# Kernel tuning notes

Measured on AMD Instinct MI355X. Metric: run time of the kernel, lower is better.

The kernel has to match this reference:

```python
import jax, jax.numpy as jnp
import numpy as np

N = 100000      # nodes
E = 1600000     # edges
H = 32          # hidden_channels
G = 512         # graphs in batch
F_IN = 7        # input node feature dim (fixed by GCNConv(7, H))
RRELU_SLOPE = (1.0 / 8.0 + 1.0 / 3.0) / 2.0  # eval-mode RReLU negative slope


def _rrelu(v):
    return jnp.where(v >= 0, v, RRELU_SLOPE * v)


def _gcn(x, row, col, ew, W, b):
    # GCNConv with normalize=True, add_self_loops=False
    deg = jax.ops.segment_sum(ew, col, num_segments=N)
    dis = jnp.where(deg > 0, jax.lax.rsqrt(deg), 0.0)
    norm = dis[row] * ew * dis[col]            # [E]
    h = x @ W                                  # [N, H]
    out = jax.ops.segment_sum(norm[:, None] * h[row], col, num_segments=N)
    return out + b


def setup_inputs() -> dict:
    key = jax.random.key(0)
    ks = jax.random.split(key, 12)
    s = 0.1
    x = jax.random.normal(ks[0], (N, F_IN), dtype=jnp.float32)
    edge_index = jax.random.randint(ks[1], (2, E), 0, N)
    batch = jnp.sort(jax.random.randint(ks[2], (N,), 0, G))
    edge_weights = jax.random.uniform(ks[3], (E,), dtype=jnp.float32)
    W1 = jax.random.normal(ks[4], (F_IN, H), dtype=jnp.float32) * s
    b1 = jnp.zeros((H,), jnp.float32)
    W2 = jax.random.normal(ks[5], (H, H), dtype=jnp.float32) * s
    b2 = jnp.zeros((H,), jnp.float32)
    Wl1 = jax.random.normal(ks[6], (H, H), dtype=jnp.float32) * s
    bl1 = jnp.zeros((H,), jnp.float32)
    Wl2 = jax.random.normal(ks[7], (H, H), dtype=jnp.float32) * s
    bl2 = jnp.zeros((H,), jnp.float32)
    Wl3 = jax.random.normal(ks[8], (H, 1), dtype=jnp.float32) * s
    bl3 = jnp.zeros((1,), jnp.float32)
    return dict(x=x, edge_index=edge_index, batch=batch, edge_weights=edge_weights,
                W1=W1, b1=b1, W2=W2, b2=b2, Wl1=Wl1, bl1=bl1, Wl2=Wl2, bl2=bl2,
                Wl3=Wl3, bl3=bl3)


def reference(x, edge_index, batch, edge_weights, W1, b1, W2, b2,
              Wl1, bl1, Wl2, bl2, Wl3, bl3):
    row, col = edge_index[0], edge_index[1]
    # conv1 (weighted GCN)
    x = _gcn(x, row, col, edge_weights, W1, b1)
    # max_pool_neighbor_x: max over incoming neighbors + self-loop
    self_idx = jnp.arange(N)
    x = jax.ops.segment_max(
        jnp.concatenate([x[row], x], axis=0),
        jnp.concatenate([col, self_idx], axis=0),
        num_segments=N)
    res = x
    # conv2 (unit edge weights)
    ones_ew = jnp.ones((E,), x.dtype)
    x = _gcn(x, row, col, ones_ew, W2, b2)
    x = jax.nn.relu(res + x)
    # global max pool over graphs
    x = jax.ops.segment_max(x, batch, num_segments=G)   # [G, H]
    res = x
    x = x @ Wl1 + bl1
    x = _rrelu(res + x)
    res = x
    x = x @ Wl2 + bl2
    x = _rrelu(res + x)
    # dropout: identity in eval mode
    x = x @ Wl3 + bl3
    return _rrelu(x)                                     # [G, 1]
```

## Files before the change

### kernel.cpp

```cpp
#include <hip/hip_runtime.h>
#include <hip/hip_bf16.h>

#define NN 100000
#define EE 1600000
#define HH 32
#define GG 512
#define FIN 7
#define NBUK 391
#define EPB 2048
#define P1G 782
#define BCAP 4608
#define SLOPE 0.22916666666666666f
#define QS 32767.0f
#define IQS (1.0f / 32767.0f)
#define RMASK 0x1FFFFu

typedef unsigned short bf16_t;
typedef unsigned int uint32;

__device__ __forceinline__ bf16_t f2b(float f) {
    return (bf16_t)(__bfloat16_as_ushort(__float2bfloat16(f)));
}
__device__ __forceinline__ float b2f(bf16_t u) {
    return __uint_as_float(((uint32)u) << 16);
}
__device__ __forceinline__ float lo16(uint32 u) { return __uint_as_float(u << 16); }
__device__ __forceinline__ float hi16(uint32 u) { return __uint_as_float(u & 0xFFFF0000u); }
__device__ __forceinline__ uint32 pack2(float a, float b) {
    return (uint32)f2b(a) | ((uint32)f2b(b) << 16);
}

__global__ __launch_bounds__(256) void k_p1(const int* __restrict__ row,
                                            const int* __restrict__ col,
                                            const float* __restrict__ ew,
                                            int* __restrict__ gcur,
                                            uint32* __restrict__ pay,
                                            unsigned char* __restrict__ nlo) {
    __shared__ int hist[NBUK];
    __shared__ int base[NBUK];
    int t = threadIdx.x;
    for (int i = t; i < NBUK; i += 256) hist[i] = 0;
    __syncthreads();
    int e0 = blockIdx.x * EPB;
    int e1 = min(e0 + EPB, EE);
    for (int e = e0 + t; e < e1; e += 256) atomicAdd(&hist[col[e] >> 8], 1);
    __syncthreads();
    for (int i = t; i < NBUK; i += 256) {
        int h = hist[i];
        base[i] = h > 0 ? atomicAdd(&gcur[i], h) : 0;
        hist[i] = 0;
    }
    __syncthreads();
    for (int e = e0 + t; e < e1; e += 256) {
        int c = col[e];
        int b = c >> 8;
        int r = atomicAdd(&hist[b], 1);
        int idx = base[b] + r;
        if (idx < BCAP) {
            size_t pos = (size_t)b * BCAP + idx;
            uint32 q = (uint32)(ew[e] * QS + 0.5f);
            pay[pos] = (q << 17) | (uint32)row[e];
            nlo[pos] = (unsigned char)(c & 255);
        }
    }
}

__global__ __launch_bounds__(512) void k_scanb(const int* __restrict__ gcur,
                                               int* __restrict__ gbase) {
    __shared__ int s[512];
    int t = threadIdx.x;
    int v = (t < NBUK) ? min(gcur[t], BCAP) : 0;
    s[t] = v;
    __syncthreads();
#pragma unroll
    for (int d = 1; d < 512; d <<= 1) {
        int u = (t >= d) ? s[t - d] : 0;
        __syncthreads();
        s[t] += u;
        __syncthreads();
    }
    if (t < NBUK) gbase[t] = s[t] - v;
}

__global__ __launch_bounds__(256) void k_p2(const int* __restrict__ gcur,
                                            const int* __restrict__ gbase,
                                            const uint32* __restrict__ pay,
                                            const unsigned char* __restrict__ nlo,
                                            const float* __restrict__ x,
                                            uint32* __restrict__ spack,
                                            int* __restrict__ cnt,
                                            int* __restrict__ off,
                                            float* __restrict__ d1s,
                                            float* __restrict__ d2,
                                            uint32* __restrict__ xsu) {
    __shared__ int hist[256];
    __shared__ int s[256];
    __shared__ int cur[256];
    __shared__ int qsum[256];
    int b = blockIdx.x, t = threadIdx.x;
    int M = min(gcur[b], BCAP);
    const uint32* bp = pay + (size_t)b * BCAP;
    const unsigned char* bn = nlo + (size_t)b * BCAP;
    hist[t] = 0;
    qsum[t] = 0;
    __syncthreads();
    for (int j = t; j < M; j += 256) atomicAdd(&hist[bn[j]], 1);
    __syncthreads();
    int v = hist[t];
    s[t] = v;
    __syncthreads();
#pragma unroll
    for (int d = 1; d < 256; d <<= 1) {
        int u = (t >= d) ? s[t - d] : 0;
        __syncthreads();
        s[t] += u;
        __syncthreads();
    }
    int excl = s[t] - v;
    int gb = gbase[b];
    int n = b * 256 + t;
    if (n < NN) { cnt[n] = v; off[n] = gb + excl; }
    cur[t] = excl;
    __syncthreads();
    for (int j = t; j < M; j += 256) {
        uint32 p = bp[j];
        unsigned char nb = bn[j];
        int r = atomicAdd(&cur[nb], 1);
        spack[gb + r] = p;
        atomicAdd(&qsum[nb], (int)(p >> 17));
    }
    __syncthreads();
    if (n < NN) {
        int sq = qsum[t];
        float dis1 = sq > 0 ? rsqrtf((float)sq * IQS) : 0.0f;
        d1s[n] = dis1 * IQS;
        d2[n] = v > 0 ? rsqrtf((float)v) : 0.0f;
        float f0 = x[n * FIN + 0] * dis1, f1 = x[n * FIN + 1] * dis1;
        float f2 = x[n * FIN + 2] * dis1, f3 = x[n * FIN + 3] * dis1;
        float f4 = x[n * FIN + 4] * dis1, f5 = x[n * FIN + 5] * dis1;
        float f6 = x[n * FIN + 6] * dis1;
        xsu[n * 4 + 0] = pack2(f0, f1);
        xsu[n * 4 + 1] = pack2(f2, f3);
        xsu[n * 4 + 2] = pack2(f4, f5);
        xsu[n * 4 + 3] = pack2(f6, 0.0f);
    }
}

__global__ __launch_bounds__(256) void k_agg1(const int* __restrict__ off,
                                              const int* __restrict__ cnt,
                                              const uint32* __restrict__ spack,
                                              const uint4* __restrict__ XS,
                                              const float* __restrict__ d1s,
                                              const float* __restrict__ b1,
                                              const float* __restrict__ W1,
                                              uint32* __restrict__ x1u) {
    __shared__ float sW[FIN * HH];
    int t = threadIdx.x;
    if (t < FIN * HH) sW[t] = W1[t];
    __syncthreads();
    int n = blockIdx.x * 16 + (t >> 4);
    int l = t & 15;
    int o = off[n], m = cnt[n];
    const uint32* bin = spack + o;
    float a0 = 0, a1 = 0, a2 = 0, a3 = 0, a4 = 0, a5 = 0, a6 = 0;
    for (int j = l; j < m; j += 16) {
        uint32 p = bin[j];
        uint4 v = XS[p & RMASK];
        float q = (float)(p >> 17);
        a0 += q * lo16(v.x); a1 += q * hi16(v.x);
        a2 += q * lo16(v.y); a3 += q * hi16(v.y);
        a4 += q * lo16(v.z); a5 += q * hi16(v.z);
        a6 += q * lo16(v.w);
    }
#pragma unroll
    for (int q = 8; q >= 1; q >>= 1) {
        a0 += __shfl_xor(a0, q, 16); a1 += __shfl_xor(a1, q, 16);
        a2 += __shfl_xor(a2, q, 16); a3 += __shfl_xor(a3, q, 16);
        a4 += __shfl_xor(a4, q, 16); a5 += __shfl_xor(a5, q, 16);
        a6 += __shfl_xor(a6, q, 16);
    }
    float sc = d1s[n];
    int c0 = 2 * l, c1 = 2 * l + 1;
    float s0 = a0 * sW[c0] + a1 * sW[HH + c0] + a2 * sW[2 * HH + c0]
             + a3 * sW[3 * HH + c0] + a4 * sW[4 * HH + c0]
             + a5 * sW[5 * HH + c0] + a6 * sW[6 * HH + c0];
    float s1 = a0 * sW[c1] + a1 * sW[HH + c1] + a2 * sW[2 * HH + c1]
             + a3 * sW[3 * HH + c1] + a4 * sW[4 * HH + c1]
             + a5 * sW[5 * HH + c1] + a6 * sW[6 * HH + c1];
    x1u[n * 16 + l] = pack2(sc * s0 + b1[c0], sc * s1 + b1[c1]);
}

__global__ __launch_bounds__(256) void k_pool(const int* __restrict__ off,
                                              const int* __restrict__ cnt,
                                              const uint32* __restrict__ spack,
                                              const uint32* __restrict__ X1,
                                              const float* __restrict__ d2,
                                              uint32* __restrict__ xpu,
                                              uint32* __restrict__ xpsu) {
    int t = threadIdx.x;
    int n = blockIdx.x * 16 + (t >> 4);
    int cp = t & 15;
    int o = off[n], m = cnt[n];
    const uint32* bin = spack + o;
    uint32 self = X1[n * 16 + cp];
    float m0 = lo16(self), m1 = hi16(self);
    int j = 0;
    for (; j + 3 < m; j += 4) {
        uint32 u0 = X1[(bin[j] & RMASK) * 16 + cp];
        uint32 u1 = X1[(bin[j + 1] & RMASK) * 16 + cp];
        uint32 u2 = X1[(bin[j + 2] & RMASK) * 16 + cp];
        uint32 u3 = X1[(bin[j + 3] & RMASK) * 16 + cp];
        m0 = fmaxf(fmaxf(m0, lo16(u0)), fmaxf(lo16(u1), fmaxf(lo16(u2), lo16(u3))));
        m1 = fmaxf(fmaxf(m1, hi16(u0)), fmaxf(hi16(u1), fmaxf(hi16(u2), hi16(u3))));
    }
    for (; j < m; j++) {
        uint32 u0 = X1[(bin[j] & RMASK) * 16 + cp];
        m0 = fmaxf(m0, lo16(u0));
        m1 = fmaxf(m1, hi16(u0));
    }
    float dn = d2[n];
    xpu[n * 16 + cp] = pack2(m0, m1);
    xpsu[n * 16 + cp] = pack2(dn * m0, dn * m1);
}

__global__ __launch_bounds__(256) void k_agg2(const int* __restrict__ off,
                                              const int* __restrict__ cnt,
                                              const uint32* __restrict__ spack,
                                              const uint32* __restrict__ XPS,
                                              float2* __restrict__ SO) {
    int t = threadIdx.x;
    int n = blockIdx.x * 16 + (t >> 4);
    int cp = t & 15;
    int o = off[n], m = cnt[n];
    const uint32* bin = spack + o;
    float a0 = 0.0f, a1 = 0.0f;
    int j = 0;
    for (; j + 3 < m; j += 4) {
        uint32 u0 = XPS[(bin[j] & RMASK) * 16 + cp];
        uint32 u1 = XPS[(bin[j + 1] & RMASK) * 16 + cp];
        uint32 u2 = XPS[(bin[j + 2] & RMASK) * 16 + cp];
        uint32 u3 = XPS[(bin[j + 3] & RMASK) * 16 + cp];
        a0 += lo16(u0) + lo16(u1) + lo16(u2) + lo16(u3);
        a1 += hi16(u0) + hi16(u1) + hi16(u2) + hi16(u3);
    }
    for (; j < m; j++) {
        uint32 u0 = XPS[(bin[j] & RMASK) * 16 + cp];
        a0 += lo16(u0);
        a1 += hi16(u0);
    }
    SO[n * 16 + cp] = make_float2(a0, a1);
}

__global__ __launch_bounds__(256) void k_xn(const float* __restrict__ Sf,
                                            const uint32* __restrict__ xpu,
                                            const float* __restrict__ d2,
                                            const float* __restrict__ b2,
                                            const float* __restrict__ W2,
                                            bf16_t* __restrict__ xnh) {
    __shared__ float sW[HH * HH];
    __shared__ float sx[8][HH];
    int t = threadIdx.x;
    for (int j = t; j < HH * HH; j += 256) sW[j] = W2[j];
    int n = blockIdx.x * 8 + (t >> 5);
    int c = t & 31, w = t >> 5;
    sx[w][c] = Sf[n * HH + c];
    __syncthreads();
    const float* xr = sx[w];
    float acc = 0.0f;
#pragma unroll
    for (int k = 0; k < HH; k++) acc += xr[k] * sW[k * HH + c];
    uint32 u = xpu[n * 16 + (c >> 1)];
    float xpv = (c & 1) ? hi16(u) : lo16(u);
    xnh[n * HH + c] = f2b(fmaxf(xpv + d2[n] * acc + b2[c], 0.0f));
}

__global__ __launch_bounds__(256) void k_gpool_mlp(const bf16_t* __restrict__ xnh,
                                                   const int* __restrict__ batch,
                                                   const float* __restrict__ Wl1,
                                                   const float* __restrict__ bl1,
                                                   const float* __restrict__ Wl2,
                                                   const float* __restrict__ bl2,
                                                   const float* __restrict__ Wl3,
                                                   const float* __restrict__ bl3,
                                                   float* __restrict__ out) {
    __shared__ float sW1[HH * HH];
    __shared__ float sW2[HH * HH];
    __shared__ float sW3[HH];
    __shared__ float sred[8][HH];
    int t = threadIdx.x;
    int g = blockIdx.x;
    for (int j = t; j < HH * HH; j += 256) {
        sW1[j] = Wl1[j];
        sW2[j] = Wl2[j];
    }
    if (t < HH) sW3[t] = Wl3[t];

    int lo = 0, hi = NN;
    while (lo < hi) { int mid = (lo + hi) >> 1; if (batch[mid] < g) lo = mid + 1; else hi = mid; }
    int s = lo;
    hi = NN;
    while (lo < hi) { int mid = (lo + hi) >> 1; if (batch[mid] < g + 1) lo = mid + 1; else hi = mid; }
    int e = lo;

    int c = t & 31, w = t >> 5;
    float mx = -3.0e38f;
    for (int i = s + w; i < e; i += 8) mx = fmaxf(mx, b2f(xnh[i * HH + c]));
    sred[w][c] = mx;
    __syncthreads();

    if (t < HH) {
        float x0 = sred[0][t];
#pragma unroll
        for (int q = 1; q < 8; q++) x0 = fmaxf(x0, sred[q][t]);
        float acc = 0.0f;
#pragma unroll
        for (int k = 0; k < HH; k++) acc += __shfl(x0, k, 32) * sW1[k * HH + t];
        float a1 = x0 + acc + bl1[t];
        a1 = a1 >= 0.0f ? a1 : SLOPE * a1;
        float acc2 = 0.0f;
#pragma unroll
        for (int k = 0; k < HH; k++) acc2 += __shfl(a1, k, 32) * sW2[k * HH + t];
        float a2 = a1 + acc2 + bl2[t];
        a2 = a2 >= 0.0f ? a2 : SLOPE * a2;
        float p = a2 * sW3[t];
#pragma unroll
        for (int o = 16; o >= 1; o >>= 1) p += __shfl_down(p, o, 32);
        if (t == 0) {
            float o = p + bl3[0];
            o = o >= 0.0f ? o : SLOPE * o;
            out[g] = o;
        }
    }
}

extern "C" void kernel_launch(void* const* d_in, const int* in_sizes, int n_in,
                              void* d_out, int out_size, void* d_ws, size_t ws_size,
                              hipStream_t stream) {
    const float* x   = (const float*)d_in[0];
    const int*   ei  = (const int*)d_in[1];
    const int*   bat = (const int*)d_in[2];
    const float* ew  = (const float*)d_in[3];
    const float* W1  = (const float*)d_in[4];
    const float* b1  = (const float*)d_in[5];
    const float* W2  = (const float*)d_in[6];
    const float* b2  = (const float*)d_in[7];
    const float* Wl1 = (const float*)d_in[8];
    const float* bl1 = (const float*)d_in[9];
    const float* Wl2 = (const float*)d_in[10];
    const float* bl2 = (const float*)d_in[11];
    const float* Wl3 = (const float*)d_in[12];
    const float* bl3 = (const float*)d_in[13];
    float* out = (float*)d_out;

    const int* row = ei;
    const int* col = ei + EE;

    char* w = (char*)d_ws;
    uint32* spack = (uint32*)w;  w += (size_t)EE * 4;
    uint32* pay   = (uint32*)w;  w += (size_t)NBUK * BCAP * 4;
    int*    gcur  = (int*)w;     w += NBUK * 4;
    int*    gbase = (int*)w;     w += NBUK * 4;
    int*    cnt   = (int*)w;     w += NN * 4;
    int*    off   = (int*)w;     w += NN * 4;
    float*  d1s   = (float*)w;   w += NN * 4;
    float*  d2    = (float*)w;   w += NN * 4;
    uint32* xsu   = (uint32*)w;  w += (size_t)NN * 4 * 4;
    uint32* x1u   = (uint32*)w;  w += (size_t)NN * 16 * 4;
    uint32* xpu   = (uint32*)w;  w += (size_t)NN * 16 * 4;
    uint32* xpsu  = (uint32*)w;  w += (size_t)NN * 16 * 4;
    float*  Sf    = (float*)w;   w += (size_t)NN * HH * 4;
    bf16_t* xnh   = (bf16_t*)w;  w += (size_t)NN * HH * 2;
    unsigned char* nlo = (unsigned char*)w;  w += (size_t)NBUK * BCAP;

    hipMemsetAsync(gcur, 0, NBUK * sizeof(int), stream);

    k_p1    <<<P1G, 256, 0, stream>>>(row, col, ew, gcur, pay, nlo);
    k_scanb <<<1, 512, 0, stream>>>(gcur, gbase);
    k_p2    <<<NBUK, 256, 0, stream>>>(gcur, gbase, pay, nlo, x, spack, cnt, off, d1s, d2, xsu);
    k_agg1  <<<NN / 16, 256, 0, stream>>>(off, cnt, spack, (const uint4*)xsu, d1s, b1, W1, x1u);
    k_pool  <<<NN / 16, 256, 0, stream>>>(off, cnt, spack, x1u, d2, xpu, xpsu);
    k_agg2  <<<NN / 16, 256, 0, stream>>>(off, cnt, spack, xpsu, (float2*)Sf);
    k_xn    <<<NN / 8, 256, 0, stream>>>(Sf, xpu, d2, b2, W2, xnh);
    k_gpool_mlp<<<GG, 256, 0, stream>>>(xnh, bat, Wl1, bl1, Wl2, bl2, Wl3, bl3, out);
}
```

Measured before the change: 275.6 us.

## Deterministic block-local binning and 16-byte wide-gather pool/agg2 kernels

The edge bucketing pass no longer takes global atomic bucket slots. Each block now sorts its edges locally by bucket into a per-block region, packing row, weight and local column into 64-bit words, and records per-block bucket offsets in a matrix. The second pass gathers each bucket's segments from every block into shared memory. This removes the memset, the scan kernel and the global atomics, but k_p2 now does serial per-segment copy loops and holds a large shared-memory array. Separately, the pool and agg2 kernels now use 64 lanes per node, each loading a 16-byte chunk for one of 16 edges, with results combined by wavefront shuffle reductions. This gives more memory-level parallelism per node, but launches four times as many blocks.

```diff
diff --git a/kernel.cpp b/kernel.cpp
--- a/kernel.cpp
+++ b/kernel.cpp
@@ -17,6 +17,7 @@
 
 typedef unsigned short bf16_t;
 typedef unsigned int uint32;
+typedef unsigned long long uint64;
 
 __device__ __forceinline__ bf16_t f2b(float f) {
     return (bf16_t)(__bfloat16_as_ushort(__float2bfloat16(f)));
@@ -33,59 +34,40 @@
 __global__ __launch_bounds__(256) void k_p1(const int* __restrict__ row,
                                             const int* __restrict__ col,
                                             const float* __restrict__ ew,
-                                            int* __restrict__ gcur,
-                                            uint32* __restrict__ pay,
-                                            unsigned char* __restrict__ nlo) {
-    __shared__ int hist[NBUK];
-    __shared__ int base[NBUK];
-    int t = threadIdx.x;
-    for (int i = t; i < NBUK; i += 256) hist[i] = 0;
-    __syncthreads();
-    int e0 = blockIdx.x * EPB;
-    int e1 = min(e0 + EPB, EE);
-    for (int e = e0 + t; e < e1; e += 256) atomicAdd(&hist[col[e] >> 8], 1);
-    __syncthreads();
-    for (int i = t; i < NBUK; i += 256) {
-        int h = hist[i];
-        base[i] = h > 0 ? atomicAdd(&gcur[i], h) : 0;
-        hist[i] = 0;
-    }
-    __syncthreads();
+                                            int* __restrict__ Pmat,
+                                            uint64* __restrict__ pay) {
+    __shared__ int h[512];
+    __shared__ int cur[392];
+    int t = threadIdx.x;
+    h[t] = 0; h[t + 256] = 0;
+    __syncthreads();
+    int e0 = blockIdx.x * EPB, e1 = min(e0 + EPB, EE);
+    for (int e = e0 + t; e < e1; e += 256) atomicAdd(&h[col[e] >> 8], 1);
+    __syncthreads();
+    int c0 = h[t], c1 = h[t + 256];
+    for (int d = 1; d < 512; d <<= 1) {
+        int a = (t >= d) ? h[t - d] : 0;
+        int b = h[t + 256 - d];
+        __syncthreads();
+        h[t] += a; h[t + 256] += b;
+        __syncthreads();
+    }
+    int ex0 = h[t] - c0, ex1 = h[t + 256] - c1;
+    if (t < 392) { cur[t] = ex0; Pmat[blockIdx.x * 392 + t] = ex0; }
+    if (t + 256 < 392) { cur[t + 256] = ex1; Pmat[blockIdx.x * 392 + t + 256] = ex1; }
+    __syncthreads();
+    uint64* bpay = pay + (size_t)blockIdx.x * EPB;
     for (int e = e0 + t; e < e1; e += 256) {
         int c = col[e];
         int b = c >> 8;
-        int r = atomicAdd(&hist[b], 1);
-        int idx = base[b] + r;
-        if (idx < BCAP) {
-            size_t pos = (size_t)b * BCAP + idx;
-            uint32 q = (uint32)(ew[e] * QS + 0.5f);
-            pay[pos] = (q << 17) | (uint32)row[e];
-            nlo[pos] = (unsigned char)(c & 255);
-        }
-    }
-}
-
-__global__ __launch_bounds__(512) void k_scanb(const int* __restrict__ gcur,
-                                               int* __restrict__ gbase) {
-    __shared__ int s[512];
-    int t = threadIdx.x;
-    int v = (t < NBUK) ? min(gcur[t], BCAP) : 0;
-    s[t] = v;
-    __syncthreads();
-#pragma unroll
-    for (int d = 1; d < 512; d <<= 1) {
-        int u = (t >= d) ? s[t - d] : 0;
-        __syncthreads();
-        s[t] += u;
-        __syncthreads();
-    }
-    if (t < NBUK) gbase[t] = s[t] - v;
-}
-
-__global__ __launch_bounds__(256) void k_p2(const int* __restrict__ gcur,
-                                            const int* __restrict__ gbase,
-                                            const uint32* __restrict__ pay,
-                                            const unsigned char* __restrict__ nlo,
+        uint32 q = (uint32)(ew[e] * QS + 0.5f);
+        int r = atomicAdd(&cur[b], 1);
+        bpay[r] = ((uint64)(uint32)(c & 255) << 32) | ((uint64)q << 17) | (uint32)row[e];
+    }
+}
+
+__global__ __launch_bounds__(256) void k_p2(const int* __restrict__ Pmat,
+                                            const uint64* __restrict__ pay,
                                             const float* __restrict__ x,
                                             uint32* __restrict__ spack,
                                             int* __restrict__ cnt,
@@ -93,23 +75,29 @@
                                             float* __restrict__ d1s,
                                             float* __restrict__ d2,
                                             uint32* __restrict__ xsu) {
-    __shared__ int hist[256];
-    __shared__ int s[256];
-    __shared__ int cur[256];
-    __shared__ int qsum[256];
+    __shared__ uint64 staged[BCAP];
+    __shared__ int hist[256], s[256], cur[256], qsum[256];
+    __shared__ int tot;
     int b = blockIdx.x, t = threadIdx.x;
-    int M = min(gcur[b], BCAP);
-    const uint32* bp = pay + (size_t)b * BCAP;
-    const unsigned char* bn = nlo + (size_t)b * BCAP;
-    hist[t] = 0;
-    qsum[t] = 0;
-    __syncthreads();
-    for (int j = t; j < M; j += 256) atomicAdd(&hist[bn[j]], 1);
-    __syncthreads();
-    int v = hist[t];
-    s[t] = v;
-    __syncthreads();
-#pragma unroll
+    hist[t] = 0; qsum[t] = 0;
+    if (t == 0) tot = 0;
+    __syncthreads();
+    for (int k = t; k < P1G; k += 256) {
+        int s0 = Pmat[k * 392 + b];
+        int s1 = Pmat[k * 392 + b + 1];
+        int len = s1 - s0;
+        if (len > 0) {
+            int r0 = atomicAdd(&tot, len);
+            const uint64* src = pay + (size_t)k * EPB + s0;
+            for (int i = 0; i < len && r0 + i < BCAP; i++) staged[r0 + i] = src[i];
+        }
+    }
+    __syncthreads();
+    int M = min(tot, BCAP);
+    for (int j = t; j < M; j += 256) atomicAdd(&hist[(int)(staged[j] >> 32)], 1);
+    __syncthreads();
+    int v = hist[t]; s[t] = v;
+    __syncthreads();
     for (int d = 1; d < 256; d <<= 1) {
         int u = (t >= d) ? s[t - d] : 0;
         __syncthreads();
@@ -117,17 +105,17 @@
         __syncthreads();
     }
     int excl = s[t] - v;
-    int gb = gbase[b];
+    int gb = b * BCAP;
     int n = b * 256 + t;
     if (n < NN) { cnt[n] = v; off[n] = gb + excl; }
     cur[t] = excl;
     __syncthreads();
     for (int j = t; j < M; j += 256) {
-        uint32 p = bp[j];
-        unsigned char nb = bn[j];
+        uint64 p = staged[j];
+        int nb = (int)(p >> 32);
         int r = atomicAdd(&cur[nb], 1);
-        spack[gb + r] = p;
-        atomicAdd(&qsum[nb], (int)(p >> 17));
+        spack[gb + r] = (uint32)p;
+        atomicAdd(&qsum[nb], (int)((uint32)p >> 17));
     }
     __syncthreads();
     if (n < NN) {
@@ -198,57 +186,83 @@
                                               uint32* __restrict__ xpu,
                                               uint32* __restrict__ xpsu) {
     int t = threadIdx.x;
-    int n = blockIdx.x * 16 + (t >> 4);
-    int cp = t & 15;
+    int n = blockIdx.x * 4 + (t >> 6);
+    int l = t & 63;
+    int eg = l >> 2, qt = l & 3;
     int o = off[n], m = cnt[n];
     const uint32* bin = spack + o;
-    uint32 self = X1[n * 16 + cp];
-    float m0 = lo16(self), m1 = hi16(self);
-    int j = 0;
-    for (; j + 3 < m; j += 4) {
-        uint32 u0 = X1[(bin[j] & RMASK) * 16 + cp];
-        uint32 u1 = X1[(bin[j + 1] & RMASK) * 16 + cp];
-        uint32 u2 = X1[(bin[j + 2] & RMASK) * 16 + cp];
-        uint32 u3 = X1[(bin[j + 3] & RMASK) * 16 + cp];
-        m0 = fmaxf(fmaxf(m0, lo16(u0)), fmaxf(lo16(u1), fmaxf(lo16(u2), lo16(u3))));
-        m1 = fmaxf(fmaxf(m1, hi16(u0)), fmaxf(hi16(u1), fmaxf(hi16(u2), hi16(u3))));
-    }
-    for (; j < m; j++) {
-        uint32 u0 = X1[(bin[j] & RMASK) * 16 + cp];
-        m0 = fmaxf(m0, lo16(u0));
-        m1 = fmaxf(m1, hi16(u0));
-    }
-    float dn = d2[n];
-    xpu[n * 16 + cp] = pack2(m0, m1);
-    xpsu[n * 16 + cp] = pack2(dn * m0, dn * m1);
+    const uint4* X4 = (const uint4*)X1;
+    uint4 u = X4[n * 4 + qt];
+    float m0 = lo16(u.x), m1 = hi16(u.x), m2 = lo16(u.y), m3 = hi16(u.y);
+    float m4 = lo16(u.z), m5 = hi16(u.z), m6 = lo16(u.w), m7 = hi16(u.w);
+    for (int j0 = 0; j0 < m; j0 += 16) {
+        int j = j0 + eg;
+        int r = (j < m) ? (int)(bin[j] & RMASK) : n;
+        uint4 v = X4[r * 4 + qt];
+        m0 = fmaxf(m0, lo16(v.x)); m1 = fmaxf(m1, hi16(v.x));
+        m2 = fmaxf(m2, lo16(v.y)); m3 = fmaxf(m3, hi16(v.y));
+        m4 = fmaxf(m4, lo16(v.z)); m5 = fmaxf(m5, hi16(v.z));
+        m6 = fmaxf(m6, lo16(v.w)); m7 = fmaxf(m7, hi16(v.w));
+    }
+#pragma unroll
+    for (int o2 = 4; o2 < 64; o2 <<= 1) {
+        m0 = fmaxf(m0, __shfl_xor(m0, o2, 64));
+        m1 = fmaxf(m1, __shfl_xor(m1, o2, 64));
+        m2 = fmaxf(m2, __shfl_xor(m2, o2, 64));
+        m3 = fmaxf(m3, __shfl_xor(m3, o2, 64));
+        m4 = fmaxf(m4, __shfl_xor(m4, o2, 64));
+        m5 = fmaxf(m5, __shfl_xor(m5, o2, 64));
+        m6 = fmaxf(m6, __shfl_xor(m6, o2, 64));
+        m7 = fmaxf(m7, __shfl_xor(m7, o2, 64));
+    }
+    if (eg == 0) {
+        float dn = d2[n];
+        uint4 w0, w1;
+        w0.x = pack2(m0, m1); w0.y = pack2(m2, m3);
+        w0.z = pack2(m4, m5); w0.w = pack2(m6, m7);
+        w1.x = pack2(dn * m0, dn * m1); w1.y = pack2(dn * m2, dn * m3);
+        w1.z = pack2(dn * m4, dn * m5); w1.w = pack2(dn * m6, dn * m7);
+        ((uint4*)xpu)[n * 4 + qt] = w0;
+        ((uint4*)xpsu)[n * 4 + qt] = w1;
+    }
 }
 
 __global__ __launch_bounds__(256) void k_agg2(const int* __restrict__ off,
                                               const int* __restrict__ cnt,
                                               const uint32* __restrict__ spack,
                                               const uint32* __restrict__ XPS,
-                                              float2* __restrict__ SO) {
-    int t = threadIdx.x;
-    int n = blockIdx.x * 16 + (t >> 4);
-    int cp = t & 15;
+                                              float* __restrict__ Sf) {
+    int t = threadIdx.x;
+    int n = blockIdx.x * 4 + (t >> 6);
+    int l = t & 63;
+    int eg = l >> 2, qt = l & 3;
     int o = off[n], m = cnt[n];
     const uint32* bin = spack + o;
-    float a0 = 0.0f, a1 = 0.0f;
-    int j = 0;
-    for (; j + 3 < m; j += 4) {
-        uint32 u0 = XPS[(bin[j] & RMASK) * 16 + cp];
-        uint32 u1 = XPS[(bin[j + 1] & RMASK) * 16 + cp];
-        uint32 u2 = XPS[(bin[j + 2] & RMASK) * 16 + cp];
-        uint32 u3 = XPS[(bin[j + 3] & RMASK) * 16 + cp];
-        a0 += lo16(u0) + lo16(u1) + lo16(u2) + lo16(u3);
-        a1 += hi16(u0) + hi16(u1) + hi16(u2) + hi16(u3);
-    }
-    for (; j < m; j++) {
-        uint32 u0 = XPS[(bin[j] & RMASK) * 16 + cp];
-        a0 += lo16(u0);
-        a1 += hi16(u0);
-    }
-    SO[n * 16 + cp] = make_float2(a0, a1);
+    const uint4* X4 = (const uint4*)XPS;
+    float a0 = 0, a1 = 0, a2 = 0, a3 = 0, a4 = 0, a5 = 0, a6 = 0, a7 = 0;
+    for (int j0 = 0; j0 < m; j0 += 16) {
+        int j = j0 + eg;
+        if (j < m) {
+            uint4 v = X4[(bin[j] & RMASK) * 4 + qt];
+            a0 += lo16(v.x); a1 += hi16(v.x);
+            a2 += lo16(v.y); a3 += hi16(v.y);
+            a4 += lo16(v.z); a5 += hi16(v.z);
+            a6 += lo16(v.w); a7 += hi16(v.w);
+        }
+    }
+#pragma unroll
+    for (int o2 = 4; o2 < 64; o2 <<= 1) {
+        a0 += __shfl_xor(a0, o2, 64); a1 += __shfl_xor(a1, o2, 64);
+        a2 += __shfl_xor(a2, o2, 64); a3 += __shfl_xor(a3, o2, 64);
+        a4 += __shfl_xor(a4, o2, 64); a5 += __shfl_xor(a5, o2, 64);
+        a6 += __shfl_xor(a6, o2, 64); a7 += __shfl_xor(a7, o2, 64);
+    }
+    if (eg == 0) {
+        float4 f0 = make_float4(a0, a1, a2, a3);
+        float4 f1 = make_float4(a4, a5, a6, a7);
+        ((float4*)Sf)[n * 8 + qt * 2] = f0;
+        ((float4*)Sf)[n * 8 + qt * 2 + 1] = f1;
+    }
 }
 
 __global__ __launch_bounds__(256) void k_xn(const float* __restrict__ Sf,
@@ -356,30 +370,25 @@
     const int* col = ei + EE;
 
     char* w = (char*)d_ws;
-    uint32* spack = (uint32*)w;  w += (size_t)EE * 4;
-    uint32* pay   = (uint32*)w;  w += (size_t)NBUK * BCAP * 4;
-    int*    gcur  = (int*)w;     w += NBUK * 4;
-    int*    gbase = (int*)w;     w += NBUK * 4;
-    int*    cnt   = (int*)w;     w += NN * 4;
-    int*    off   = (int*)w;     w += NN * 4;
-    float*  d1s   = (float*)w;   w += NN * 4;
-    float*  d2    = (float*)w;   w += NN * 4;
-    uint32* xsu   = (uint32*)w;  w += (size_t)NN * 4 * 4;
-    uint32* x1u   = (uint32*)w;  w += (size_t)NN * 16 * 4;
-    uint32* xpu   = (uint32*)w;  w += (size_t)NN * 16 * 4;
-    uint32* xpsu  = (uint32*)w;  w += (size_t)NN * 16 * 4;
-    float*  Sf    = (float*)w;   w += (size_t)NN * HH * 4;
-    bf16_t* xnh   = (bf16_t*)w;  w += (size_t)NN * HH * 2;
-    unsigned char* nlo = (unsigned char*)w;  w += (size_t)NBUK * BCAP;
-
-    hipMemsetAsync(gcur, 0, NBUK * sizeof(int), stream);
-
-    k_p1    <<<P1G, 256, 0, stream>>>(row, col, ew, gcur, pay, nlo);
-    k_scanb <<<1, 512, 0, stream>>>(gcur, gbase);
-    k_p2    <<<NBUK, 256, 0, stream>>>(gcur, gbase, pay, nlo, x, spack, cnt, off, d1s, d2, xsu);
-    k_agg1  <<<NN / 16, 256, 0, stream>>>(off, cnt, spack, (const uint4*)xsu, d1s, b1, W1, x1u);
-    k_pool  <<<NN / 16, 256, 0, stream>>>(off, cnt, spack, x1u, d2, xpu, xpsu);
-    k_agg2  <<<NN / 16, 256, 0, stream>>>(off, cnt, spack, xpsu, (float2*)Sf);
-    k_xn    <<<NN / 8, 256, 0, stream>>>(Sf, xpu, d2, b2, W2, xnh);
+    uint64* pay  = (uint64*)w;  w += (size_t)P1G * EPB * 8;
+    float*  Sf   = (float*)pay;
+    int*   Pmat  = (int*)w;     w += (size_t)P1G * 392 * 4;
+    uint32* spack = (uint32*)w; w += (size_t)NBUK * BCAP * 4;
+    int*    cnt  = (int*)w;     w += NN * 4;
+    int*    off  = (int*)w;     w += NN * 4;
+    float*  d1s  = (float*)w;   w += NN * 4;
+    float*  d2   = (float*)w;   w += NN * 4;
+    uint32* xsu  = (uint32*)w;  w += (size_t)NN * 4 * 4;
+    uint32* x1u  = (uint32*)w;  w += (size_t)NN * 16 * 4;
+    uint32* xpu  = (uint32*)w;  w += (size_t)NN * 16 * 4;
+    uint32* xpsu = (uint32*)w;  w += (size_t)NN * 16 * 4;
+    bf16_t* xnh  = (bf16_t*)w;  w += (size_t)NN * HH * 2;
+
+    k_p1   <<<P1G, 256, 0, stream>>>(row, col, ew, Pmat, pay);
+    k_p2   <<<NBUK, 256, 0, stream>>>(Pmat, pay, x, spack, cnt, off, d1s, d2, xsu);
+    k_agg1 <<<NN / 16, 256, 0, stream>>>(off, cnt, spack, (const uint4*)xsu, d1s, b1, W1, x1u);
+    k_pool <<<NN / 4, 256, 0, stream>>>(off, cnt, spack, x1u, d2, xpu, xpsu);
+    k_agg2 <<<NN / 4, 256, 0, stream>>>(off, cnt, spack, xpsu, Sf);
+    k_xn   <<<NN / 8, 256, 0, stream>>>(Sf, xpu, d2, b2, W2, xnh);
     k_gpool_mlp<<<GG, 256, 0, stream>>>(xnh, bat, Wl1, bl1, Wl2, bl2, Wl3, bl3, out);
 }
```

Result: no change. 273.5 us (-0.8%).
